# Kernel optimization log

Hardware: AMD Instinct MI355X
Metric: run time of the kernel (lower is better)

The kernel has to match this reference:

```python
import jax, jax.numpy as jnp
import numpy as np

EPS = 1e-12  # torch F.normalize eps

def l2norm(x, axis):
    n = jnp.sqrt(jnp.sum(x * x, axis=axis, keepdims=True))
    return x / jnp.maximum(n, EPS)

def setup_inputs() -> dict:
    key = jax.random.key(0)
    k1, k2, k3, k4 = jax.random.split(key, 4)
    N, C, H, W, K = 128, 128, 64, 64, 64
    x = jax.random.normal(k1, (N, C, H, W), dtype=jnp.float32)
    conv_w = jax.random.normal(k2, (K, C), dtype=jnp.float32) * 0.1
    conv_b = jax.random.normal(k3, (K,), dtype=jnp.float32) * 0.1
    centroids = jax.random.uniform(k4, (K, C), dtype=jnp.float32)
    return {"x": x, "conv_w": conv_w, "conv_b": conv_b, "centroids": centroids}

def reference(x, conv_w, conv_b, centroids):
    N, C, H, W = x.shape
    K = centroids.shape[0]
    xf = x.reshape(N, C, H * W)               # [N, C, S]
    xf = l2norm(xf, axis=1)                   # normalize_input over channels
    # 1x1 conv -> logits [N, K, S], softmax over clusters
    logits = jnp.einsum('ncs,kc->nks', xf, conv_w) + conv_b[None, :, None]
    a = jax.nn.softmax(logits, axis=1)        # [N, K, S]
    # VLAD: sum_s a[n,k,s]*(x[n,:,s] - c[k]) = (a @ x^T) - (sum_s a) * c
    vlad = jnp.einsum('nks,ncs->nkc', a, xf) - a.sum(axis=-1)[:, :, None] * centroids[None]
    vlad = l2norm(vlad, axis=2)               # intra-normalization
    vlad = vlad.reshape(N, K * C)
    return l2norm(vlad, axis=1)
```

## Files before the change

### kernel.cpp

```cpp
#include <hip/hip_runtime.h>
#include <math.h>

#define N_IMG 128
#define C_DIM 128
#define K_CL  64
#define S_PIX 4096
#define PB    8
#define SPB   (S_PIX/PB)
#define CHK   64
#define NCHK  (SPB/CHK)
#define SROW  72
#define ASZ   (K_CL*SROW)
#define NBUF  3

#define KXOR(c) ((((c)&3)<<2) | (((c)>>2)&3))

typedef __attribute__((ext_vector_type(8))) short bf16x8;
typedef __attribute__((ext_vector_type(4))) float f32x4;

__device__ __forceinline__ unsigned short f2bf_rn(float v) {
    unsigned u = __float_as_uint(v);
    unsigned r = u + 0x7fffu + ((u >> 16) & 1u);
    return (unsigned short)(r >> 16);
}
__device__ __forceinline__ float bf2f(unsigned short h) {
    return __uint_as_float(((unsigned)h) << 16);
}

__device__ __forceinline__ void cvt8(const float* v, bf16x8& h, bf16x8& l) {
    union { unsigned w[4]; bf16x8 v8; } H, L;
    #pragma unroll
    for (int p = 0; p < 4; ++p) {
        unsigned u0 = __float_as_uint(v[2*p]);
        unsigned u1 = __float_as_uint(v[2*p+1]);
        float r0 = v[2*p]   - __uint_as_float(u0 & 0xffff0000u);
        float r1 = v[2*p+1] - __uint_as_float(u1 & 0xffff0000u);
        H.w[p] = __builtin_amdgcn_perm(u1, u0, 0x07060302u);
        L.w[p] = __builtin_amdgcn_perm(__float_as_uint(r1), __float_as_uint(r0), 0x07060302u);
    }
    h = H.v8; l = L.v8;
}

__device__ __forceinline__ void gll16(const float* g, float* l) {
    __builtin_amdgcn_global_load_lds(
        (const __attribute__((address_space(1))) unsigned int*)(g),
        (__attribute__((address_space(3))) unsigned int*)(l),
        16, 0, 0);
}

__global__ void k_prep(const float* __restrict__ w, unsigned short* __restrict__ wf) {
    int i = blockIdx.x * 256 + threadIdx.x;
    int j = i & 7, l = (i >> 3) & 63, t = (i >> 9) & 3, m = (i >> 11) & 3;
    int k = 16*m + (l & 15);
    int c = 32*t + 4*j + (l >> 4);
    float v = w[k * C_DIM + c];
    unsigned short h = f2bf_rn(v);
    wf[i]        = h;
    wf[8192 + i] = f2bf_rn(v - bf2f(h));
}

__global__ void k_clear(float4* __restrict__ out4, float4* __restrict__ asum4) {
    int i = blockIdx.x * 256 + threadIdx.x;
    f32x4 z = (f32x4)0.f;
    if (i < (N_IMG*K_CL*C_DIM)/4) out4[i] = *(float4*)&z;
    if (i < (N_IMG*K_CL)/4)       asum4[i] = *(float4*)&z;
}

__global__ __launch_bounds__(512, 1)
void k_main(const float* __restrict__ x,
            const unsigned short* __restrict__ wf,
            const float* __restrict__ bias,
            float* __restrict__ vlad,
            float* __restrict__ asum)
{
    __shared__ float Xs[NBUF][C_DIM*CHK/2];
    __shared__ float Xs2[NBUF][C_DIM*CHK - C_DIM*CHK/2];
    __shared__ unsigned short aS[2*ASZ];
    __shared__ float redS[4][2][16];

    auto XP = [&](int b, int idx) -> float* {
        return (idx < 4096) ? &Xs[b][idx] : &Xs2[b][idx - 4096];
    };

    const int tid  = threadIdx.x;
    const int lane = tid & 63;
    const int wid  = tid >> 6;
    const int lc   = lane & 15;
    const int g    = lane >> 4;

    const int p  = wid & 3;
    const int mh = wid >> 2;
    const int px = p*16 + lc;
    const int cq = wid * 16;

    const int n  = blockIdx.x / PB;
    const int sp = blockIdx.x % PB;
    const float* xn = x + (size_t)n * (C_DIM * S_PIX) + sp * SPB;

    bf16x8 Wh[2][4], Wl[2][4];
    #pragma unroll
    for (int mm = 0; mm < 2; ++mm)
        #pragma unroll
        for (int t = 0; t < 4; ++t) {
            int m = 2*mh + mm;
            Wh[mm][t] = *(const bf16x8*)&wf[((m*4 + t)*64 + lane)*8];
            Wl[mm][t] = *(const bf16x8*)&wf[((16 + m*4 + t)*64 + lane)*8];
        }
    #pragma unroll
    for (int mm = 0; mm < 2; ++mm)
        #pragma unroll
        for (int t = 0; t < 4; ++t) {
            asm volatile("" : "+v"(Wh[mm][t]));
            asm volatile("" : "+v"(Wl[mm][t]));
        }

    f32x4 bias_r[2];
    #pragma unroll
    for (int mm = 0; mm < 2; ++mm)
        bias_r[mm] = *(const f32x4*)&bias[32*mh + 16*mm + 4*g];

    f32x4 accV[4];
    #pragma unroll
    for (int m = 0; m < 4; ++m) accV[m] = (f32x4)0.f;
    float asum_acc[8];
    #pragma unroll
    for (int i = 0; i < 8; ++i) asum_acc[i] = 0.f;

    const int r0 = wid * 16;

    auto STAGE = [&](int t, int b) {
        #pragma unroll
        for (int i2 = 0; i2 < 4; ++i2) {
            int rowbase = r0 + i2*4;
            int row = rowbase + (lane >> 4);
            const float* gp = xn + (size_t)row * S_PIX + t*CHK
                            + 4*((lane & 15) ^ KXOR(row));
            gll16(gp, XP(b, rowbase * 64));
        }
    };

    STAGE(0, 0);
    STAGE(1, 1);
    asm volatile("s_waitcnt vmcnt(4)" ::: "memory");
    __builtin_amdgcn_s_barrier();
    __builtin_amdgcn_sched_barrier(0);

    #pragma unroll
    for (int ch = 0; ch < NCHK; ++ch) {
        const int rb = ch % NBUF;

        if (ch + 2 < NCHK) STAGE(ch + 2, (ch + 2) % NBUF);

        float ss = 0.f;
        f32x4 accL[2];
        accL[0] = (f32x4)0.f; accL[1] = (f32x4)0.f;
        #pragma unroll
        for (int t = 0; t < 4; ++t) {
            float xv[8];
            #pragma unroll
            for (int j = 0; j < 8; ++j) {
                int c = 32*t + 4*j + g;
                xv[j] = *XP(rb, c*64 + 4*((px>>2) ^ KXOR(c)) + (px&3));
            }
            #pragma unroll
            for (int j = 0; j < 8; ++j) ss = fmaf(xv[j], xv[j], ss);
            bf16x8 xh, xl;
            cvt8(xv, xh, xl);
            #pragma unroll
            for (int mm = 0; mm < 2; ++mm) {
                accL[mm] = __builtin_amdgcn_mfma_f32_16x16x32_bf16(Wh[mm][t], xh, accL[mm], 0,0,0);
                accL[mm] = __builtin_amdgcn_mfma_f32_16x16x32_bf16(Wh[mm][t], xl, accL[mm], 0,0,0);
                accL[mm] = __builtin_amdgcn_mfma_f32_16x16x32_bf16(Wl[mm][t], xh, accL[mm], 0,0,0);
            }
        }
        ss += __shfl_xor(ss, 16); ss += __shfl_xor(ss, 32);
        float rnorm = 1.0f / fmaxf(sqrtf(ss), 1e-12f);

        float e[8]; float sm = 0.f;
        #pragma unroll
        for (int mm = 0; mm < 2; ++mm)
            #pragma unroll
            for (int jj = 0; jj < 4; ++jj) {
                float t2 = __expf(fmaf(accL[mm][jj], rnorm, bias_r[mm][jj]));
                e[mm*4+jj] = t2;
                sm += t2;
            }
        sm += __shfl_xor(sm, 16); sm += __shfl_xor(sm, 32);
        if (g == 0) redS[p][mh][lc] = sm;

        asm volatile("s_waitcnt lgkmcnt(0)" ::: "memory");
        __builtin_amdgcn_s_barrier();
        __builtin_amdgcn_sched_barrier(0);

        float S = sm + redS[p][mh^1][lc];
        float coef  = 1.0f / S;
        float coefr = coef * rnorm;

        #pragma unroll
        for (int mm = 0; mm < 2; ++mm)
            #pragma unroll
            for (int jj = 0; jj < 4; ++jj) {
                float ev = e[mm*4+jj];
                asum_acc[mm*4+jj] += ev * coef;
                float ap = ev * coefr;
                unsigned u = __float_as_uint(ap);
                float r = ap - __uint_as_float(u & 0xffff0000u);
                int k = 32*mh + 16*mm + 4*g + jj;
                int ix = k*SROW + px;
                aS[ix]       = (unsigned short)(u >> 16);
                aS[ASZ + ix] = (unsigned short)(__float_as_uint(r) >> 16);
            }

        asm volatile("s_waitcnt lgkmcnt(0)" ::: "memory");
        __builtin_amdgcn_s_barrier();
        __builtin_amdgcn_sched_barrier(0);

        #pragma unroll
        for (int ks = 0; ks < 2; ++ks) {
            bf16x8 Ah[4], Al[4];
            #pragma unroll
            for (int m = 0; m < 4; ++m) {
                int off = (16*m + lc)*SROW + ks*32 + 8*g;
                Ah[m] = *(const bf16x8*)&aS[off];
                Al[m] = *(const bf16x8*)&aS[ASZ + off];
            }
            int c  = cq + lc;
            int s0 = 8*ks + 2*g;
            float4 f0 = *(const float4*)XP(rb, c*64 + 4*((s0)   ^ KXOR(c)));
            float4 f1 = *(const float4*)XP(rb, c*64 + 4*((s0+1) ^ KXOR(c)));
            float xv[8] = {f0.x,f0.y,f0.z,f0.w,f1.x,f1.y,f1.z,f1.w};
            bf16x8 xh, xl;
            cvt8(xv, xh, xl);
            #pragma unroll
            for (int m = 0; m < 4; ++m) {
                accV[m] = __builtin_amdgcn_mfma_f32_16x16x32_bf16(Ah[m], xh, accV[m], 0,0,0);
                accV[m] = __builtin_amdgcn_mfma_f32_16x16x32_bf16(Ah[m], xl, accV[m], 0,0,0);
                accV[m] = __builtin_amdgcn_mfma_f32_16x16x32_bf16(Al[m], xh, accV[m], 0,0,0);
            }
        }

        if (ch < NCHK - 1) {
            if (ch + 2 < NCHK) asm volatile("s_waitcnt vmcnt(4)" ::: "memory");
            else               asm volatile("s_waitcnt vmcnt(0)" ::: "memory");
            __builtin_amdgcn_s_barrier();
            __builtin_amdgcn_sched_barrier(0);
        }
    }

    float* vb = vlad + (size_t)n * (K_CL * C_DIM);
    #pragma unroll
    for (int m = 0; m < 4; ++m)
        #pragma unroll
        for (int jj = 0; jj < 4; ++jj)
            atomicAdd(&vb[(16*m + 4*g + jj)*C_DIM + cq + lc], accV[m][jj]);

    #pragma unroll
    for (int i = 0; i < 8; ++i) {
        float v = asum_acc[i];
        v += __shfl_xor(v, 1); v += __shfl_xor(v, 2);
        v += __shfl_xor(v, 4); v += __shfl_xor(v, 8);
        asum_acc[i] = v;
    }
    if (lc == 0) {
        #pragma unroll
        for (int mm = 0; mm < 2; ++mm)
            #pragma unroll
            for (int jj = 0; jj < 4; ++jj)
                atomicAdd(&asum[n*K_CL + 32*mh + 16*mm + 4*g + jj], asum_acc[mm*4+jj]);
    }
}

__global__ __launch_bounds__(256)
void k_final(float* __restrict__ vlad,
             const float* __restrict__ asum,
             const float* __restrict__ cent)
{
    __shared__ float v[K_CL * 132];
    __shared__ float red[K_CL][4];
    __shared__ float rin[K_CL];
    __shared__ float rtot_s;
    const int tid = threadIdx.x;
    const int n   = blockIdx.x;
    float* vb = vlad + (size_t)n * (K_CL * C_DIM);
    const float* as = asum + n * K_CL;

    for (int i = tid; i < K_CL*C_DIM; i += 256) {
        int k = i >> 7, c = i & 127;
        v[k*132 + c] = vb[i] - as[k] * cent[i];
    }
    __syncthreads();
    {
        int k = tid >> 2, p = tid & 3;
        float s2 = 0.f;
        #pragma unroll
        for (int u = 0; u < 32; ++u) { float t = v[k*132 + (u<<2) + p]; s2 = fmaf(t, t, s2); }
        red[k][p] = s2;
    }
    __syncthreads();
    if (tid < K_CL) {
        float s2 = red[tid][0] + red[tid][1] + red[tid][2] + red[tid][3];
        float r  = 1.0f / fmaxf(sqrtf(s2), 1e-12f);
        rin[tid] = r;
        red[tid][0] = s2 * r * r;
    }
    __syncthreads();
    if (tid < 64) {
        float t = red[tid][0];
        t += __shfl_xor(t, 32); t += __shfl_xor(t, 16); t += __shfl_xor(t, 8);
        t += __shfl_xor(t, 4);  t += __shfl_xor(t, 2);  t += __shfl_xor(t, 1);
        if (tid == 0) rtot_s = 1.0f / fmaxf(sqrtf(t), 1e-12f);
    }
    __syncthreads();
    float rt = rtot_s;
    for (int i = tid; i < K_CL*C_DIM; i += 256) {
        vb[i] = v[(i>>7)*132 + (i&127)] * rin[i>>7] * rt;
    }
}

extern "C" void kernel_launch(void* const* d_in, const int* in_sizes, int n_in,
                              void* d_out, int out_size, void* d_ws, size_t ws_size,
                              hipStream_t stream) {
    const float* x    = (const float*)d_in[0];
    const float* w    = (const float*)d_in[1];
    const float* b    = (const float*)d_in[2];
    const float* cent = (const float*)d_in[3];
    float* out = (float*)d_out;
    unsigned short* wf = (unsigned short*)d_ws;
    float* asum = (float*)((char*)d_ws + 32768);

    k_clear<<<(N_IMG*K_CL*C_DIM/4 + 255)/256, 256, 0, stream>>>(
        (float4*)out, (float4*)asum);
    k_prep<<<32, 256, 0, stream>>>(w, wf);
    k_main<<<N_IMG * PB, 512, 0, stream>>>(x, wf, b, out, asum);
    k_final<<<N_IMG, 256, 0, stream>>>(out, asum, cent);
}
```

Measured before the change: 128.4 us.

## Halve chunk size and re-split logits work across waves to raise occupancy

Shrinks the per-chunk pixel tile from 64 to 32, so LDS use per block drops and launch bounds allow up to 4 blocks per CU instead of 1. The logits work is re-split: each wave now handles 16 clusters for 16 pixels rather than 32 clusters for 16 pixels, which halves the weight registers per wave. The softmax reduction therefore combines four partial sums instead of two. The XOR swizzles for the X tile and the A tile are rewritten for the new row widths. In exchange there are twice as many chunks, so twice as many barriers per block.

```diff
diff --git a/kernel.cpp b/kernel.cpp
--- a/kernel.cpp
+++ b/kernel.cpp
@@ -7,13 +7,11 @@
 #define S_PIX 4096
 #define PB    8
 #define SPB   (S_PIX/PB)
-#define CHK   64
+#define CHK   32
 #define NCHK  (SPB/CHK)
-#define SROW  72
-#define ASZ   (K_CL*SROW)
 #define NBUF  3
-
-#define KXOR(c) ((((c)&3)<<2) | (((c)>>2)&3))
+#define AROW  64
+#define APL   (K_CL*AROW)
 
 typedef __attribute__((ext_vector_type(8))) short bf16x8;
 typedef __attribute__((ext_vector_type(4))) float f32x4;
@@ -46,6 +44,10 @@
         (const __attribute__((address_space(1))) unsigned int*)(g),
         (__attribute__((address_space(3))) unsigned int*)(l),
         16, 0, 0);
+}
+
+__device__ __forceinline__ int a_slot(int k, int g8) {
+    return 4*(k & 1) + (g8 ^ ((k >> 1) & 3));
 }
 
 __global__ void k_prep(const float* __restrict__ w, unsigned short* __restrict__ wf) {
@@ -66,21 +68,16 @@
     if (i < (N_IMG*K_CL)/4)       asum4[i] = *(float4*)&z;
 }
 
-__global__ __launch_bounds__(512, 1)
+__global__ __launch_bounds__(512, 4)
 void k_main(const float* __restrict__ x,
             const unsigned short* __restrict__ wf,
             const float* __restrict__ bias,
             float* __restrict__ vlad,
             float* __restrict__ asum)
 {
-    __shared__ float Xs[NBUF][C_DIM*CHK/2];
-    __shared__ float Xs2[NBUF][C_DIM*CHK - C_DIM*CHK/2];
-    __shared__ unsigned short aS[2*ASZ];
-    __shared__ float redS[4][2][16];
-
-    auto XP = [&](int b, int idx) -> float* {
-        return (idx < 4096) ? &Xs[b][idx] : &Xs2[b][idx - 4096];
-    };
+    __shared__ float Xs[NBUF][C_DIM*CHK];
+    __shared__ unsigned short aS[2*APL];
+    __shared__ float redS[2][4][16];
 
     const int tid  = threadIdx.x;
     const int lane = tid & 63;
@@ -88,8 +85,8 @@
     const int lc   = lane & 15;
     const int g    = lane >> 4;
 
-    const int p  = wid & 3;
-    const int mh = wid >> 2;
+    const int p  = wid & 1;
+    const int q  = wid >> 1;
     const int px = p*16 + lc;
     const int cq = wid * 16;
 
@@ -97,137 +94,118 @@
     const int sp = blockIdx.x % PB;
     const float* xn = x + (size_t)n * (C_DIM * S_PIX) + sp * SPB;
 
-    bf16x8 Wh[2][4], Wl[2][4];
-    #pragma unroll
-    for (int mm = 0; mm < 2; ++mm)
-        #pragma unroll
-        for (int t = 0; t < 4; ++t) {
-            int m = 2*mh + mm;
-            Wh[mm][t] = *(const bf16x8*)&wf[((m*4 + t)*64 + lane)*8];
-            Wl[mm][t] = *(const bf16x8*)&wf[((16 + m*4 + t)*64 + lane)*8];
-        }
-    #pragma unroll
-    for (int mm = 0; mm < 2; ++mm)
-        #pragma unroll
-        for (int t = 0; t < 4; ++t) {
-            asm volatile("" : "+v"(Wh[mm][t]));
-            asm volatile("" : "+v"(Wl[mm][t]));
-        }
-
-    f32x4 bias_r[2];
-    #pragma unroll
-    for (int mm = 0; mm < 2; ++mm)
-        bias_r[mm] = *(const f32x4*)&bias[32*mh + 16*mm + 4*g];
+    bf16x8 Wh[4], Wl[4];
+    #pragma unroll
+    for (int t = 0; t < 4; ++t) {
+        Wh[t] = *(const bf16x8*)&wf[((q*4 + t)*64 + lane)*8];
+        Wl[t] = *(const bf16x8*)&wf[((16 + q*4 + t)*64 + lane)*8];
+    }
+    #pragma unroll
+    for (int t = 0; t < 4; ++t) {
+        asm volatile("" : "+v"(Wh[t]));
+        asm volatile("" : "+v"(Wl[t]));
+    }
+    f32x4 bias_r = *(const f32x4*)&bias[16*q + 4*g];
 
     f32x4 accV[4];
     #pragma unroll
     for (int m = 0; m < 4; ++m) accV[m] = (f32x4)0.f;
-    float asum_acc[8];
-    #pragma unroll
-    for (int i = 0; i < 8; ++i) asum_acc[i] = 0.f;
+    float asum_acc[4] = {0.f, 0.f, 0.f, 0.f};
 
     const int r0 = wid * 16;
 
     auto STAGE = [&](int t, int b) {
         #pragma unroll
-        for (int i2 = 0; i2 < 4; ++i2) {
-            int rowbase = r0 + i2*4;
-            int row = rowbase + (lane >> 4);
+        for (int h = 0; h < 2; ++h) {
+            int rowbase = r0 + h*8;
+            int row = rowbase + (lane >> 3);
             const float* gp = xn + (size_t)row * S_PIX + t*CHK
-                            + 4*((lane & 15) ^ KXOR(row));
-            gll16(gp, XP(b, rowbase * 64));
+                            + 4*((lane & 7) ^ (row & 7));
+            gll16(gp, &Xs[b][rowbase * 32]);
         }
     };
 
     STAGE(0, 0);
     STAGE(1, 1);
-    asm volatile("s_waitcnt vmcnt(4)" ::: "memory");
+    asm volatile("s_waitcnt vmcnt(2)" ::: "memory");
     __builtin_amdgcn_s_barrier();
     __builtin_amdgcn_sched_barrier(0);
 
     #pragma unroll
     for (int ch = 0; ch < NCHK; ++ch) {
         const int rb = ch % NBUF;
+        const float* Xb = &Xs[rb][0];
 
         if (ch + 2 < NCHK) STAGE(ch + 2, (ch + 2) % NBUF);
 
         float ss = 0.f;
-        f32x4 accL[2];
-        accL[0] = (f32x4)0.f; accL[1] = (f32x4)0.f;
+        f32x4 accL = (f32x4)0.f;
         #pragma unroll
         for (int t = 0; t < 4; ++t) {
             float xv[8];
             #pragma unroll
             for (int j = 0; j < 8; ++j) {
                 int c = 32*t + 4*j + g;
-                xv[j] = *XP(rb, c*64 + 4*((px>>2) ^ KXOR(c)) + (px&3));
+                xv[j] = Xb[c*32 + (((px>>2) ^ (c&7)) << 2) + (px&3)];
             }
             #pragma unroll
             for (int j = 0; j < 8; ++j) ss = fmaf(xv[j], xv[j], ss);
             bf16x8 xh, xl;
             cvt8(xv, xh, xl);
-            #pragma unroll
-            for (int mm = 0; mm < 2; ++mm) {
-                accL[mm] = __builtin_amdgcn_mfma_f32_16x16x32_bf16(Wh[mm][t], xh, accL[mm], 0,0,0);
-                accL[mm] = __builtin_amdgcn_mfma_f32_16x16x32_bf16(Wh[mm][t], xl, accL[mm], 0,0,0);
-                accL[mm] = __builtin_amdgcn_mfma_f32_16x16x32_bf16(Wl[mm][t], xh, accL[mm], 0,0,0);
-            }
+            accL = __builtin_amdgcn_mfma_f32_16x16x32_bf16(Wh[t], xh, accL, 0,0,0);
+            accL = __builtin_amdgcn_mfma_f32_16x16x32_bf16(Wh[t], xl, accL, 0,0,0);
+            accL = __builtin_amdgcn_mfma_f32_16x16x32_bf16(Wl[t], xh, accL, 0,0,0);
         }
         ss += __shfl_xor(ss, 16); ss += __shfl_xor(ss, 32);
         float rnorm = 1.0f / fmaxf(sqrtf(ss), 1e-12f);
 
-        float e[8]; float sm = 0.f;
-        #pragma unroll
-        for (int mm = 0; mm < 2; ++mm)
-            #pragma unroll
-            for (int jj = 0; jj < 4; ++jj) {
-                float t2 = __expf(fmaf(accL[mm][jj], rnorm, bias_r[mm][jj]));
-                e[mm*4+jj] = t2;
-                sm += t2;
-            }
+        float e[4]; float sm = 0.f;
+        #pragma unroll
+        for (int jj = 0; jj < 4; ++jj) {
+            float t2 = __expf(fmaf(accL[jj], rnorm, bias_r[jj]));
+            e[jj] = t2;
+            sm += t2;
+        }
         sm += __shfl_xor(sm, 16); sm += __shfl_xor(sm, 32);
-        if (g == 0) redS[p][mh][lc] = sm;
+        if (g == 0) redS[p][q][lc] = sm;
 
         asm volatile("s_waitcnt lgkmcnt(0)" ::: "memory");
         __builtin_amdgcn_s_barrier();
         __builtin_amdgcn_sched_barrier(0);
 
-        float S = sm + redS[p][mh^1][lc];
+        float S = redS[p][0][lc] + redS[p][1][lc] + redS[p][2][lc] + redS[p][3][lc];
         float coef  = 1.0f / S;
         float coefr = coef * rnorm;
 
         #pragma unroll
-        for (int mm = 0; mm < 2; ++mm)
-            #pragma unroll
-            for (int jj = 0; jj < 4; ++jj) {
-                float ev = e[mm*4+jj];
-                asum_acc[mm*4+jj] += ev * coef;
-                float ap = ev * coefr;
-                unsigned u = __float_as_uint(ap);
-                float r = ap - __uint_as_float(u & 0xffff0000u);
-                int k = 32*mh + 16*mm + 4*g + jj;
-                int ix = k*SROW + px;
-                aS[ix]       = (unsigned short)(u >> 16);
-                aS[ASZ + ix] = (unsigned short)(__float_as_uint(r) >> 16);
-            }
+        for (int jj = 0; jj < 4; ++jj) {
+            float ev = e[jj];
+            asum_acc[jj] += ev * coef;
+            float ap = ev * coefr;
+            unsigned u = __float_as_uint(ap);
+            float r = ap - __uint_as_float(u & 0xffff0000u);
+            int k = 16*q + 4*g + jj;
+            int ix = k*AROW + a_slot(k, px>>3)*8 + (px&7);
+            aS[ix]       = (unsigned short)(u >> 16);
+            aS[APL + ix] = (unsigned short)(__float_as_uint(r) >> 16);
+        }
 
         asm volatile("s_waitcnt lgkmcnt(0)" ::: "memory");
         __builtin_amdgcn_s_barrier();
         __builtin_amdgcn_sched_barrier(0);
 
-        #pragma unroll
-        for (int ks = 0; ks < 2; ++ks) {
+        {
             bf16x8 Ah[4], Al[4];
             #pragma unroll
             for (int m = 0; m < 4; ++m) {
-                int off = (16*m + lc)*SROW + ks*32 + 8*g;
+                int k = 16*m + lc;
+                int off = k*AROW + a_slot(k, g)*8;
                 Ah[m] = *(const bf16x8*)&aS[off];
-                Al[m] = *(const bf16x8*)&aS[ASZ + off];
+                Al[m] = *(const bf16x8*)&aS[APL + off];
             }
-            int c  = cq + lc;
-            int s0 = 8*ks + 2*g;
-            float4 f0 = *(const float4*)XP(rb, c*64 + 4*((s0)   ^ KXOR(c)));
-            float4 f1 = *(const float4*)XP(rb, c*64 + 4*((s0+1) ^ KXOR(c)));
+            int c = cq + lc;
+            float4 f0 = *(const float4*)&Xb[c*32 + (((2*g)   ^ (c&7)) << 2)];
+            float4 f1 = *(const float4*)&Xb[c*32 + (((2*g+1) ^ (c&7)) << 2)];
             float xv[8] = {f0.x,f0.y,f0.z,f0.w,f1.x,f1.y,f1.z,f1.w};
             bf16x8 xh, xl;
             cvt8(xv, xh, xl);
@@ -240,7 +218,7 @@
         }
 
         if (ch < NCHK - 1) {
-            if (ch + 2 < NCHK) asm volatile("s_waitcnt vmcnt(4)" ::: "memory");
+            if (ch + 2 < NCHK) asm volatile("s_waitcnt vmcnt(2)" ::: "memory");
             else               asm volatile("s_waitcnt vmcnt(0)" ::: "memory");
             __builtin_amdgcn_s_barrier();
             __builtin_amdgcn_sched_barrier(0);
@@ -255,7 +233,7 @@
             atomicAdd(&vb[(16*m + 4*g + jj)*C_DIM + cq + lc], accV[m][jj]);
 
     #pragma unroll
-    for (int i = 0; i < 8; ++i) {
+    for (int i = 0; i < 4; ++i) {
         float v = asum_acc[i];
         v += __shfl_xor(v, 1); v += __shfl_xor(v, 2);
         v += __shfl_xor(v, 4); v += __shfl_xor(v, 8);
@@ -263,10 +241,8 @@
     }
     if (lc == 0) {
         #pragma unroll
-        for (int mm = 0; mm < 2; ++mm)
-            #pragma unroll
-            for (int jj = 0; jj < 4; ++jj)
-                atomicAdd(&asum[n*K_CL + 32*mh + 16*mm + 4*g + jj], asum_acc[mm*4+jj]);
+        for (int jj = 0; jj < 4; ++jj)
+            atomicAdd(&asum[n*K_CL + 16*q + 4*g + jj], asum_acc[jj]);
     }
 }
 
```

Measured after the change: 165.4 us. 28.8% more time.

## Halve block size and chunk width, deepen pipeline to four buffers

Applied to the files above, without the earlier changes.

Moves k_main from 512-thread blocks with 64-pixel chunks and three LDS buffers to 256-thread blocks with 32-pixel chunks, four buffers (prefetch distance 3) and launch_bounds(256,2), so two blocks can share a CU. Each wave now covers 32 channels in the VLAD MFMA stage, with new XOR swizzles for the X and assignment tiles in LDS. The intent is better latency hiding through more resident blocks and a deeper prefetch. In exchange there are twice as many chunk iterations, each paying barrier overhead, and higher register pressure from the doubled accumulators.

```diff
diff --git a/kernel.cpp b/kernel.cpp
--- a/kernel.cpp
+++ b/kernel.cpp
@@ -7,13 +7,9 @@
 #define S_PIX 4096
 #define PB    8
 #define SPB   (S_PIX/PB)
-#define CHK   64
+#define CHK   32
 #define NCHK  (SPB/CHK)
-#define SROW  72
-#define ASZ   (K_CL*SROW)
-#define NBUF  3
-
-#define KXOR(c) ((((c)&3)<<2) | (((c)>>2)&3))
+#define NBUF  4
 
 typedef __attribute__((ext_vector_type(8))) short bf16x8;
 typedef __attribute__((ext_vector_type(4))) float f32x4;
@@ -26,6 +22,9 @@
 __device__ __forceinline__ float bf2f(unsigned short h) {
     return __uint_as_float(((unsigned)h) << 16);
 }
+
+__device__ __forceinline__ int sx(int c) { return ((c & 3) | ((c & 1) << 2)) & 7; }
+__device__ __forceinline__ int sa(int k) { return (k >> 2) & 3; }
 
 __device__ __forceinline__ void cvt8(const float* v, bf16x8& h, bf16x8& l) {
     union { unsigned w[4]; bf16x8 v8; } H, L;
@@ -66,21 +65,16 @@
     if (i < (N_IMG*K_CL)/4)       asum4[i] = *(float4*)&z;
 }
 
-__global__ __launch_bounds__(512, 1)
+__global__ __launch_bounds__(256, 2)
 void k_main(const float* __restrict__ x,
             const unsigned short* __restrict__ wf,
             const float* __restrict__ bias,
             float* __restrict__ vlad,
             float* __restrict__ asum)
 {
-    __shared__ float Xs[NBUF][C_DIM*CHK/2];
-    __shared__ float Xs2[NBUF][C_DIM*CHK - C_DIM*CHK/2];
-    __shared__ unsigned short aS[2*ASZ];
-    __shared__ float redS[4][2][16];
-
-    auto XP = [&](int b, int idx) -> float* {
-        return (idx < 4096) ? &Xs[b][idx] : &Xs2[b][idx - 4096];
-    };
+    __shared__ float Xs[NBUF][C_DIM*CHK];
+    __shared__ unsigned short aS[2*K_CL*CHK];
+    __shared__ float redS[2][2][16];
 
     const int tid  = threadIdx.x;
     const int lane = tid & 63;
@@ -88,10 +82,10 @@
     const int lc   = lane & 15;
     const int g    = lane >> 4;
 
-    const int p  = wid & 3;
-    const int mh = wid >> 2;
+    const int p  = wid & 1;
+    const int mh = wid >> 1;
     const int px = p*16 + lc;
-    const int cq = wid * 16;
+    const int cq = wid * 32;
 
     const int n  = blockIdx.x / PB;
     const int sp = blockIdx.x % PB;
@@ -113,43 +107,44 @@
             asm volatile("" : "+v"(Wh[mm][t]));
             asm volatile("" : "+v"(Wl[mm][t]));
         }
-
     f32x4 bias_r[2];
     #pragma unroll
     for (int mm = 0; mm < 2; ++mm)
         bias_r[mm] = *(const f32x4*)&bias[32*mh + 16*mm + 4*g];
 
-    f32x4 accV[4];
-    #pragma unroll
-    for (int m = 0; m < 4; ++m) accV[m] = (f32x4)0.f;
+    f32x4 accV[4][2];
+    #pragma unroll
+    for (int m = 0; m < 4; ++m) { accV[m][0] = (f32x4)0.f; accV[m][1] = (f32x4)0.f; }
     float asum_acc[8];
     #pragma unroll
     for (int i = 0; i < 8; ++i) asum_acc[i] = 0.f;
 
-    const int r0 = wid * 16;
-
-    auto STAGE = [&](int t, int b) {
+    const int eA  = g*32 + (((px >> 2) ^ sx(g)) << 2) + (px & 3);
+    const int sxB = sx(lc);
+    const int saB = sa(lc);
+
+    auto STAGE = [&](int t, float* Xbuf) {
         #pragma unroll
         for (int i2 = 0; i2 < 4; ++i2) {
-            int rowbase = r0 + i2*4;
-            int row = rowbase + (lane >> 4);
+            int rowblk = wid*32 + i2*8;
+            int row = rowblk + (lane >> 3);
             const float* gp = xn + (size_t)row * S_PIX + t*CHK
-                            + 4*((lane & 15) ^ KXOR(row));
-            gll16(gp, XP(b, rowbase * 64));
+                            + 4*((lane & 7) ^ sx(row));
+            gll16(gp, &Xbuf[rowblk * 32]);
         }
     };
 
-    STAGE(0, 0);
-    STAGE(1, 1);
-    asm volatile("s_waitcnt vmcnt(4)" ::: "memory");
+    STAGE(0, Xs[0]);
+    STAGE(1, Xs[1]);
+    STAGE(2, Xs[2]);
+    asm volatile("s_waitcnt vmcnt(8)" ::: "memory");
     __builtin_amdgcn_s_barrier();
     __builtin_amdgcn_sched_barrier(0);
 
-    #pragma unroll
     for (int ch = 0; ch < NCHK; ++ch) {
-        const int rb = ch % NBUF;
-
-        if (ch + 2 < NCHK) STAGE(ch + 2, (ch + 2) % NBUF);
+        float* Xb = Xs[ch & (NBUF-1)];
+
+        if (ch + 3 < NCHK) STAGE(ch + 3, Xs[(ch + 3) & (NBUF-1)]);
 
         float ss = 0.f;
         f32x4 accL[2];
@@ -158,10 +153,8 @@
         for (int t = 0; t < 4; ++t) {
             float xv[8];
             #pragma unroll
-            for (int j = 0; j < 8; ++j) {
-                int c = 32*t + 4*j + g;
-                xv[j] = *XP(rb, c*64 + 4*((px>>2) ^ KXOR(c)) + (px&3));
-            }
+            for (int j = 0; j < 8; ++j)
+                xv[j] = Xb[eA + 1024*t + 128*j];
             #pragma unroll
             for (int j = 0; j < 8; ++j) ss = fmaf(xv[j], xv[j], ss);
             bf16x8 xh, xl;
@@ -205,43 +198,49 @@
                 float ap = ev * coefr;
                 unsigned u = __float_as_uint(ap);
                 float r = ap - __uint_as_float(u & 0xffff0000u);
-                int k = 32*mh + 16*mm + 4*g + jj;
-                int ix = k*SROW + px;
-                aS[ix]       = (unsigned short)(u >> 16);
-                aS[ASZ + ix] = (unsigned short)(__float_as_uint(r) >> 16);
+                int k  = 32*mh + 16*mm + 4*g + jj;
+                int ix = k*32 + (((px >> 3) ^ g) << 3) + (px & 7);
+                aS[ix]        = (unsigned short)(u >> 16);
+                aS[2048 + ix] = (unsigned short)(__float_as_uint(r) >> 16);
             }
 
         asm volatile("s_waitcnt lgkmcnt(0)" ::: "memory");
         __builtin_amdgcn_s_barrier();
         __builtin_amdgcn_sched_barrier(0);
 
-        #pragma unroll
-        for (int ks = 0; ks < 2; ++ks) {
+        {
             bf16x8 Ah[4], Al[4];
             #pragma unroll
             for (int m = 0; m < 4; ++m) {
-                int off = (16*m + lc)*SROW + ks*32 + 8*g;
+                int off = (16*m + lc)*32 + ((g ^ saB) << 3);
                 Ah[m] = *(const bf16x8*)&aS[off];
-                Al[m] = *(const bf16x8*)&aS[ASZ + off];
-            }
-            int c  = cq + lc;
-            int s0 = 8*ks + 2*g;
-            float4 f0 = *(const float4*)XP(rb, c*64 + 4*((s0)   ^ KXOR(c)));
-            float4 f1 = *(const float4*)XP(rb, c*64 + 4*((s0+1) ^ KXOR(c)));
-            float xv[8] = {f0.x,f0.y,f0.z,f0.w,f1.x,f1.y,f1.z,f1.w};
-            bf16x8 xh, xl;
-            cvt8(xv, xh, xl);
-            #pragma unroll
-            for (int m = 0; m < 4; ++m) {
-                accV[m] = __builtin_amdgcn_mfma_f32_16x16x32_bf16(Ah[m], xh, accV[m], 0,0,0);
-                accV[m] = __builtin_amdgcn_mfma_f32_16x16x32_bf16(Ah[m], xl, accV[m], 0,0,0);
-                accV[m] = __builtin_amdgcn_mfma_f32_16x16x32_bf16(Al[m], xh, accV[m], 0,0,0);
-            }
-        }
-
-        if (ch < NCHK - 1) {
-            if (ch + 2 < NCHK) asm volatile("s_waitcnt vmcnt(4)" ::: "memory");
-            else               asm volatile("s_waitcnt vmcnt(0)" ::: "memory");
+                Al[m] = *(const bf16x8*)&aS[2048 + off];
+            }
+            #pragma unroll
+            for (int nn = 0; nn < 2; ++nn) {
+                int c  = cq + nn*16 + lc;
+                int P0 = (2*g) ^ sxB;
+                float4 f0 = *(const float4*)&Xb[c*32 + P0*4];
+                float4 f1 = *(const float4*)&Xb[c*32 + (P0 ^ 1)*4];
+                float xv[8] = {f0.x,f0.y,f0.z,f0.w,f1.x,f1.y,f1.z,f1.w};
+                bf16x8 xh, xl;
+                cvt8(xv, xh, xl);
+                #pragma unroll
+                for (int m = 0; m < 4; ++m) {
+                    accV[m][nn] = __builtin_amdgcn_mfma_f32_16x16x32_bf16(Ah[m], xh, accV[m][nn], 0,0,0);
+                    accV[m][nn] = __builtin_amdgcn_mfma_f32_16x16x32_bf16(Ah[m], xl, accV[m][nn], 0,0,0);
+                    accV[m][nn] = __builtin_amdgcn_mfma_f32_16x16x32_bf16(Al[m], xh, accV[m][nn], 0,0,0);
+                }
+            }
+        }
+
+        if (ch + 1 < NCHK) {
+            if (ch + 3 < NCHK)
+                asm volatile("s_waitcnt vmcnt(8) lgkmcnt(0)" ::: "memory");
+            else if (ch + 2 < NCHK)
+                asm volatile("s_waitcnt vmcnt(4) lgkmcnt(0)" ::: "memory");
+            else
+                asm volatile("s_waitcnt vmcnt(0) lgkmcnt(0)" ::: "memory");
             __builtin_amdgcn_s_barrier();
             __builtin_amdgcn_sched_barrier(0);
         }
@@ -251,8 +250,11 @@
     #pragma unroll
     for (int m = 0; m < 4; ++m)
         #pragma unroll
-        for (int jj = 0; jj < 4; ++jj)
-            atomicAdd(&vb[(16*m + 4*g + jj)*C_DIM + cq + lc], accV[m][jj]);
+        for (int nn = 0; nn < 2; ++nn)
+            #pragma unroll
+            for (int jj = 0; jj < 4; ++jj)
+                atomicAdd(&vb[(16*m + 4*g + jj)*C_DIM + cq + nn*16 + lc],
+                          accV[m][nn][jj]);
 
     #pragma unroll
     for (int i = 0; i < 8; ++i) {
@@ -331,6 +333,6 @@
     k_clear<<<(N_IMG*K_CL*C_DIM/4 + 255)/256, 256, 0, stream>>>(
         (float4*)out, (float4*)asum);
     k_prep<<<32, 256, 0, stream>>>(w, wf);
-    k_main<<<N_IMG * PB, 512, 0, stream>>>(x, wf, b, out, asum);
+    k_main<<<N_IMG * PB, 256, 0, stream>>>(x, wf, b, out, asum);
     k_final<<<N_IMG, 256, 0, stream>>>(out, asum, cent);
 }
```

New measurement: 115.2 us. 10.3% less time.
